# Performance work log

Hardware: AMD Instinct MI355X
Metric: run time of the kernel (lower is better)

Reference implementation:

```python
import jax, jax.numpy as jnp
import numpy as np

N = 50000
IN_C, HID_C, CLS_C = 512, 256, 128
E = 800000


def setup_inputs() -> dict:
    key = jax.random.key(0)
    k1, k2, k3, k4, k5, k6 = jax.random.split(key, 6)
    x = jax.random.normal(k1, (N, IN_C), dtype=jnp.float32)
    edge_index = jax.random.randint(k2, (2, E), 0, N, dtype=jnp.int64)
    # GCNConv params (glorot weights, zero bias as in PyG init)
    W1 = jax.random.normal(k3, (IN_C, HID_C), dtype=jnp.float32) * (1.0 / np.sqrt(IN_C))
    b1 = jnp.zeros((HID_C,), dtype=jnp.float32)
    W2 = jax.random.normal(k4, (HID_C, CLS_C), dtype=jnp.float32) * (1.0 / np.sqrt(HID_C))
    b2 = jnp.zeros((CLS_C,), dtype=jnp.float32)
    return {"x": x, "W1": W1, "b1": b1, "W2": W2, "b2": b2, "edge_index": edge_index}


def _norm_edges(edge_index, n):
    # PyG GCNConv: add self-loops, symmetric normalization deg^-1/2
    loops = jnp.arange(n, dtype=edge_index.dtype)
    src = jnp.concatenate([edge_index[0], loops])
    dst = jnp.concatenate([edge_index[1], loops])
    ones = jnp.ones_like(src, dtype=jnp.float32)
    deg = jax.ops.segment_sum(ones, dst, num_segments=n)
    dinv = jnp.where(deg > 0, jax.lax.rsqrt(deg), 0.0)
    norm = dinv[src] * dinv[dst]  # [E+N]
    return src, dst, norm


def _gcn_conv(x, W, b, src, dst, norm, n):
    h = x @ W  # project first (out_channels < in_channels)
    msg = h[src] * norm[:, None]  # gather + scale, [E+N, C]
    out = jax.ops.segment_sum(msg, dst, num_segments=n)  # scatter-add
    return out + b


def reference(x, W1, b1, W2, b2, edge_index):
    n = x.shape[0]
    src, dst, norm = _norm_edges(edge_index, n)
    h = jax.nn.relu(_gcn_conv(x, W1, b1, src, dst, norm, n))
    # dropout p=0.5 is a no-op in eval mode
    out = _gcn_conv(h, W2, b2, src, dst, norm, n)
    return jax.nn.sigmoid(out)
```

## Files before the change

kernel.cpp:

```cpp
#include <hip/hip_runtime.h>
#include <type_traits>

typedef __attribute__((ext_vector_type(8))) short bf16x8;
typedef __attribute__((ext_vector_type(4))) float f32x4;
typedef unsigned short u16;
typedef unsigned int u32;
typedef __attribute__((address_space(1))) const u32 gu32;
typedef __attribute__((address_space(3))) u32 lu32;

__device__ __forceinline__ float bf2f(u16 u) {
  union { u32 i; float f; } c; c.i = ((u32)u) << 16; return c.f;
}
__device__ __forceinline__ u16 f2bf(float f) {
  union { float f; u32 i; } c; c.f = f;
  u32 u = c.i;
  u32 r = (u + 0x7FFFu + ((u >> 16) & 1u)) >> 16;
  return (u16)r;
}

__device__ __forceinline__ void gld16(const void* g, void* l) {
  __builtin_amdgcn_global_load_lds((gu32*)g, (lu32*)l, 16, 0, 0);
}


__global__ void k_init_deg(int* deg, int n) {
  int i = blockIdx.x * 256 + threadIdx.x;
  if (i < n) deg[i] = 1;
}

__global__ void k_count(const int* __restrict__ ei, int* deg, int E) {
  int e = blockIdx.x * 256 + threadIdx.x;
  if (e < E) atomicAdd(&deg[ei[E + e]], 1);
}

__global__ void k_blocksum(const int* __restrict__ deg, int* bsum, int n) {
  __shared__ int s[256];
  int t = threadIdx.x;
  int i = blockIdx.x * 256 + t;
  s[t] = (i < n) ? (deg[i] - 1) : 0;
  __syncthreads();
  for (int o = 128; o > 0; o >>= 1) {
    if (t < o) s[t] += s[t + o];
    __syncthreads();
  }
  if (t == 0) bsum[blockIdx.x] = s[0];
}

__global__ void k_scanb(const int* __restrict__ bsum, int* bofs, int nb) {
  __shared__ int s[256];
  int t = threadIdx.x;
  int v = (t < nb) ? bsum[t] : 0;
  s[t] = v;
  __syncthreads();
  for (int o = 1; o < 256; o <<= 1) {
    int x = (t >= o) ? s[t - o] : 0;
    __syncthreads();
    s[t] += x;
    __syncthreads();
  }
  bofs[t] = s[t] - v;
}

__global__ void k_rowptr(const int* __restrict__ deg, const int* __restrict__ bofs,
                         int* rowptr, int* cursor, float* dinv, int n) {
  __shared__ int s[256];
  int t = threadIdx.x;
  int i = blockIdx.x * 256 + t;
  int d = (i < n) ? deg[i] : 1;
  int v = (i < n) ? (d - 1) : 0;
  s[t] = v;
  __syncthreads();
  for (int o = 1; o < 256; o <<= 1) {
    int x = (t >= o) ? s[t - o] : 0;
    __syncthreads();
    s[t] += x;
    __syncthreads();
  }
  int excl = s[t] - v + bofs[blockIdx.x];
  if (i < n) {
    rowptr[i] = excl;
    cursor[i] = excl;
    dinv[i] = rsqrtf((float)d);
    if (i == n - 1) rowptr[n] = excl + v;
  }
}

__global__ void k_fill(const int* __restrict__ ei, int* cursor,
                       const float* __restrict__ dinv, int2* colw, int E) {
  int e = blockIdx.x * 256 + threadIdx.x;
  if (e >= E) return;
  int s = ei[e];
  int d = ei[E + e];
  int pos = atomicAdd(&cursor[d], 1);
  colw[pos] = make_int2(s, __float_as_int(dinv[s]));
}

__global__ void k_twt(const float* __restrict__ W, u16* __restrict__ Wt, int K, int N) {
  int i = blockIdx.x * 256 + threadIdx.x;
  if (i >= K * N) return;
  int k = i / N, n = i - k * N;
  Wt[n * K + k] = f2bf(W[i]);
}


template <bool AF32, int K>
__launch_bounds__(256)
__global__ void gemm_kernel(const void* __restrict__ Ap, const u16* __restrict__ Bt,
                            u16* __restrict__ C, int M, int ldc) {
  using AT = typename std::conditional<AF32, float, u16>::type;
  __shared__ AT As_[2][4096];
  __shared__ u16 Bs_[2][4096];

  const int tid = threadIdx.x;
  const int lane = tid & 63;
  const int wid = tid >> 6;
  const int wr = wid >> 1, wc = wid & 1;
  const long brow = (long)blockIdx.x * 128;
  const long bcol = (long)blockIdx.y * 128;

  constexpr int NT = K / 32;
  constexpr int NJA = AF32 ? 4 : 2;

  const AT* agp[NJA];
  AT* alp[NJA];
#pragma unroll
  for (int j = 0; j < NJA; ++j) {
    int idx = j * 256 + tid;
    int row, u;
    if constexpr (AF32) { row = idx >> 3; u = (idx & 7) ^ (row & 7); }
    else                { row = idx >> 2; u = (idx & 3) ^ (row & 3); }
    long grow = brow + row;
    if (grow > (long)M - 1) grow = M - 1;
    agp[j] = (const AT*)Ap + grow * (long)K + u * (AF32 ? 4 : 8);
    alp[j] = &As_[0][idx * (AF32 ? 4 : 8)];
  }
  const u16* bgp[2];
  u16* blp[2];
#pragma unroll
  for (int j = 0; j < 2; ++j) {
    int idx = j * 256 + tid;
    int row = idx >> 2;
    int u = (idx & 3) ^ (row & 3);
    bgp[j] = Bt + (bcol + row) * (long)K + u * 8;
    blp[j] = &Bs_[0][idx * 8];
  }

  f32x4 acc[4][4];
#pragma unroll
  for (int i = 0; i < 4; i++)
#pragma unroll
    for (int j = 0; j < 4; j++) acc[i][j] = (f32x4){0.f, 0.f, 0.f, 0.f};

  auto stage = [&](int kt, int buf) {
    const int boff = buf * 4096;
#pragma unroll
    for (int j = 0; j < NJA; ++j) gld16(agp[j] + kt * 32, alp[j] + boff);
#pragma unroll
    for (int j = 0; j < 2; ++j) gld16(bgp[j] + kt * 32, blp[j] + boff);
  };

  stage(0, 0);
  int cur = 0;
  for (int kt = 0; kt < NT; ++kt) {
    __syncthreads();
    if (kt + 1 < NT) stage(kt + 1, cur ^ 1);

    bf16x8 af[4], bfq[4];
#pragma unroll
    for (int i = 0; i < 4; i++) {
      const int row = wr * 64 + i * 16 + (lane & 15);
      if constexpr (AF32) {
        const float* bp = (const float*)&As_[cur][0] + row * 32;
        const int s = row & 7;
        const int u0 = (lane >> 4) * 2;
        float4 x0 = *(const float4*)(bp + (u0 ^ s) * 4);
        float4 x1 = *(const float4*)(bp + ((u0 + 1) ^ s) * 4);
        union { u32 w[4]; bf16x8 v; } cv;
        asm("v_cvt_pk_bf16_f32 %0, %1, %2" : "=v"(cv.w[0]) : "v"(x0.x), "v"(x0.y));
        asm("v_cvt_pk_bf16_f32 %0, %1, %2" : "=v"(cv.w[1]) : "v"(x0.z), "v"(x0.w));
        asm("v_cvt_pk_bf16_f32 %0, %1, %2" : "=v"(cv.w[2]) : "v"(x1.x), "v"(x1.y));
        asm("v_cvt_pk_bf16_f32 %0, %1, %2" : "=v"(cv.w[3]) : "v"(x1.z), "v"(x1.w));
        af[i] = cv.v;
      } else {
        const int u = (lane >> 4) ^ (row & 3);
        af[i] = *(const bf16x8*)((const u16*)&As_[cur][0] + row * 32 + u * 8);
      }
    }
#pragma unroll
    for (int j = 0; j < 4; j++) {
      const int row = wc * 64 + j * 16 + (lane & 15);
      const int u = (lane >> 4) ^ (row & 3);
      bfq[j] = *(const bf16x8*)(&Bs_[cur][0] + row * 32 + u * 8);
    }
#pragma unroll
    for (int i = 0; i < 4; i++)
#pragma unroll
      for (int j = 0; j < 4; j++)
        acc[i][j] = __builtin_amdgcn_mfma_f32_16x16x32_bf16(af[i], bfq[j], acc[i][j], 0, 0, 0);
    cur ^= 1;
  }

#pragma unroll
  for (int i = 0; i < 4; i++) {
    const long r0 = brow + wr * 64 + i * 16 + ((lane >> 4) * 4);
#pragma unroll
    for (int j = 0; j < 4; j++) {
      const long cc = bcol + wc * 64 + j * 16 + (lane & 15);
#pragma unroll
      for (int q = 0; q < 4; q++) {
        long r = r0 + q;
        if (r < M) C[r * (long)ldc + cc] = f2bf(acc[i][j][q]);
      }
    }
  }
}


__launch_bounds__(256)
__global__ void agg1(const u16* __restrict__ h0, const int* __restrict__ rowptr,
                     const int2* __restrict__ colw, const float* __restrict__ dinv,
                     const float* __restrict__ b1, u16* __restrict__ h, int n) {
  const int wid = threadIdx.x >> 6, lane = threadIdx.x & 63;
  const int node = blockIdx.x * 4 + wid;
  if (node >= n) return;
  const float di = dinv[node];
  ushort4 sv = ((const ushort4*)(h0 + (size_t)node * 256))[lane];
  float a0 = di * bf2f(sv.x), a1 = di * bf2f(sv.y), a2 = di * bf2f(sv.z), a3 = di * bf2f(sv.w);
  int e = rowptr[node];
  const int r1 = rowptr[node + 1];
  for (; e + 4 <= r1; e += 4) {
    int2 c0 = colw[e], c1 = colw[e + 1], c2 = colw[e + 2], c3 = colw[e + 3];
    float w0 = __int_as_float(c0.y), w1 = __int_as_float(c1.y);
    float w2 = __int_as_float(c2.y), w3 = __int_as_float(c3.y);
    ushort4 v0 = ((const ushort4*)(h0 + (size_t)c0.x * 256))[lane];
    ushort4 v1 = ((const ushort4*)(h0 + (size_t)c1.x * 256))[lane];
    ushort4 v2 = ((const ushort4*)(h0 + (size_t)c2.x * 256))[lane];
    ushort4 v3 = ((const ushort4*)(h0 + (size_t)c3.x * 256))[lane];
    a0 += w0 * bf2f(v0.x) + w1 * bf2f(v1.x) + w2 * bf2f(v2.x) + w3 * bf2f(v3.x);
    a1 += w0 * bf2f(v0.y) + w1 * bf2f(v1.y) + w2 * bf2f(v2.y) + w3 * bf2f(v3.y);
    a2 += w0 * bf2f(v0.z) + w1 * bf2f(v1.z) + w2 * bf2f(v2.z) + w3 * bf2f(v3.z);
    a3 += w0 * bf2f(v0.w) + w1 * bf2f(v1.w) + w2 * bf2f(v2.w) + w3 * bf2f(v3.w);
  }
  for (; e < r1; ++e) {
    int2 c = colw[e];
    float wv = __int_as_float(c.y);
    ushort4 v = ((const ushort4*)(h0 + (size_t)c.x * 256))[lane];
    a0 += wv * bf2f(v.x); a1 += wv * bf2f(v.y); a2 += wv * bf2f(v.z); a3 += wv * bf2f(v.w);
  }
  float4 bb = ((const float4*)b1)[lane];
  a0 = a0 * di + bb.x; a1 = a1 * di + bb.y; a2 = a2 * di + bb.z; a3 = a3 * di + bb.w;
  a0 = a0 > 0.f ? a0 : 0.f; a1 = a1 > 0.f ? a1 : 0.f;
  a2 = a2 > 0.f ? a2 : 0.f; a3 = a3 > 0.f ? a3 : 0.f;
  ushort4 o; o.x = f2bf(a0); o.y = f2bf(a1); o.z = f2bf(a2); o.w = f2bf(a3);
  ((ushort4*)(h + (size_t)node * 256))[lane] = o;
}

__device__ __forceinline__ float sigmoidf_(float x) { return 1.f / (1.f + __expf(-x)); }

__launch_bounds__(256)
__global__ void agg2(const u16* __restrict__ h2, const int* __restrict__ rowptr,
                     const int2* __restrict__ colw, const float* __restrict__ dinv,
                     const float* __restrict__ b2, float* __restrict__ out, int n) {
  const int wid = threadIdx.x >> 6, lane = threadIdx.x & 63;
  const int node = blockIdx.x * 4 + wid;
  if (node >= n) return;
  const float di = dinv[node];
  ushort2 sv = ((const ushort2*)(h2 + (size_t)node * 128))[lane];
  float a0 = di * bf2f(sv.x), a1 = di * bf2f(sv.y);
  int e = rowptr[node];
  const int r1 = rowptr[node + 1];
  for (; e + 4 <= r1; e += 4) {
    int2 c0 = colw[e], c1 = colw[e + 1], c2 = colw[e + 2], c3 = colw[e + 3];
    float w0 = __int_as_float(c0.y), w1 = __int_as_float(c1.y);
    float w2 = __int_as_float(c2.y), w3 = __int_as_float(c3.y);
    ushort2 v0 = ((const ushort2*)(h2 + (size_t)c0.x * 128))[lane];
    ushort2 v1 = ((const ushort2*)(h2 + (size_t)c1.x * 128))[lane];
    ushort2 v2 = ((const ushort2*)(h2 + (size_t)c2.x * 128))[lane];
    ushort2 v3 = ((const ushort2*)(h2 + (size_t)c3.x * 128))[lane];
    a0 += w0 * bf2f(v0.x) + w1 * bf2f(v1.x) + w2 * bf2f(v2.x) + w3 * bf2f(v3.x);
    a1 += w0 * bf2f(v0.y) + w1 * bf2f(v1.y) + w2 * bf2f(v2.y) + w3 * bf2f(v3.y);
  }
  for (; e < r1; ++e) {
    int2 c = colw[e];
    float wv = __int_as_float(c.y);
    ushort2 v = ((const ushort2*)(h2 + (size_t)c.x * 128))[lane];
    a0 += wv * bf2f(v.x); a1 += wv * bf2f(v.y);
  }
  float2 bb = ((const float2*)b2)[lane];
  float2 o;
  o.x = sigmoidf_(a0 * di + bb.x);
  o.y = sigmoidf_(a1 * di + bb.y);
  ((float2*)(out + (size_t)node * 128))[lane] = o;
}


extern "C" void kernel_launch(void* const* d_in, const int* in_sizes, int n_in,
                              void* d_out, int out_size, void* d_ws, size_t ws_size,
                              hipStream_t stream) {
  const float* x  = (const float*)d_in[0];
  const float* W1 = (const float*)d_in[1];
  const float* b1 = (const float*)d_in[2];
  const float* W2 = (const float*)d_in[3];
  const float* b2 = (const float*)d_in[4];
  const int*   ei = (const int*)d_in[5];

  const int N = in_sizes[0] / 512;
  const int E = in_sizes[5] / 2;
  const int Mpad = (N + 127) & ~127;
  float* outp = (float*)d_out;

  char* w = (char*)d_ws;
  size_t off = 0;
  auto take = [&](size_t bytes) -> void* {
    void* p = w + off;
    off = (off + bytes + 255) & ~(size_t)255;
    return p;
  };
  u16*   h0     = (u16*)take((size_t)Mpad * 256 * 2);
  u16*   hb     = (u16*)take((size_t)Mpad * 256 * 2);
  u16*   h2     = (u16*)take((size_t)Mpad * 128 * 2);
  u16*   W1t    = (u16*)take(256 * 512 * 2);
  u16*   W2t    = (u16*)take(128 * 256 * 2);
  int*   deg    = (int*)take((size_t)N * 4);
  float* dinv   = (float*)take((size_t)N * 4);
  int*   rowptr = (int*)take((size_t)(N + 1) * 4);
  int*   cursor = (int*)take((size_t)N * 4);
  int2*  colw   = (int2*)take((size_t)E * 8);
  int*   bsum   = (int*)take(256 * 4);
  int*   bofs   = (int*)take(256 * 4);
  (void)ws_size; (void)n_in; (void)out_size;

  const int nb = (N + 255) / 256;
  const int eb = (E + 255) / 256;

  k_init_deg<<<nb, 256, 0, stream>>>(deg, N);
  k_count<<<eb, 256, 0, stream>>>(ei, deg, E);
  k_blocksum<<<nb, 256, 0, stream>>>(deg, bsum, N);
  k_scanb<<<1, 256, 0, stream>>>(bsum, bofs, nb);
  k_rowptr<<<nb, 256, 0, stream>>>(deg, bofs, rowptr, cursor, dinv, N);
  k_fill<<<eb, 256, 0, stream>>>(ei, cursor, dinv, colw, E);
  k_twt<<<(512 * 256 + 255) / 256, 256, 0, stream>>>(W1, W1t, 512, 256);
  k_twt<<<(256 * 128 + 255) / 256, 256, 0, stream>>>(W2, W2t, 256, 128);

  dim3 g1(Mpad / 128, 2);
  gemm_kernel<true, 512><<<g1, 256, 0, stream>>>((const void*)x, W1t, h0, N, 256);
  agg1<<<(N + 3) / 4, 256, 0, stream>>>(h0, rowptr, colw, dinv, b1, hb, N);
  dim3 g2(Mpad / 128, 1);
  gemm_kernel<false, 256><<<g2, 256, 0, stream>>>((const void*)hb, W2t, h2, Mpad, 128);
  agg2<<<(N + 3) / 4, 256, 0, stream>>>(h2, rowptr, colw, dinv, b2, outp, N);
}
```

Measured before the change: 251.9 us.

## Restructure GEMM A-staging to bf16 in LDS and column-split edge aggregation

The first GEMM now loads fp32 A tiles into registers, converts them to bf16 once, and writes them to LDS. This halves LDS footprint and replaces repeated conversions during MFMA fragment reads with a single conversion per tile. The second GEMM uses 64-row tiles to launch more blocks. Both aggregation kernels are replaced by one templated kernel that splits channels into 32-wide partitions across blocks and processes 8 edges in parallel per wave with shuffle reductions. This aims to raise memory-level parallelism and L2 locality for gathers, at the cost of reading the CSR edge lists multiple times (once per partition) and more wasted lanes on low-degree nodes.

```diff
diff --git a/kernel.cpp b/kernel.cpp
--- a/kernel.cpp
+++ b/kernel.cpp
@@ -1,5 +1,4 @@
 #include <hip/hip_runtime.h>
-#include <type_traits>
 
 typedef __attribute__((ext_vector_type(8))) short bf16x8;
 typedef __attribute__((ext_vector_type(4))) float f32x4;
@@ -103,37 +102,25 @@
 }
 
 
-template <bool AF32, int K>
-__launch_bounds__(256)
+template <bool AF32, int K, int BM>
+__launch_bounds__(256, 4)
 __global__ void gemm_kernel(const void* __restrict__ Ap, const u16* __restrict__ Bt,
                             u16* __restrict__ C, int M, int ldc) {
-  using AT = typename std::conditional<AF32, float, u16>::type;
-  __shared__ AT As_[2][4096];
+  constexpr int NT = K / 32;
+  constexpr int AE = BM * 32;
+  constexpr int WROWS = BM / 2;
+  constexpr int FI = WROWS / 16;
+  constexpr int NJA = BM / 64;
+  __shared__ u16 As_[2][AE];
   __shared__ u16 Bs_[2][4096];
 
   const int tid = threadIdx.x;
   const int lane = tid & 63;
   const int wid = tid >> 6;
   const int wr = wid >> 1, wc = wid & 1;
-  const long brow = (long)blockIdx.x * 128;
+  const long brow = (long)blockIdx.x * BM;
   const long bcol = (long)blockIdx.y * 128;
 
-  constexpr int NT = K / 32;
-  constexpr int NJA = AF32 ? 4 : 2;
-
-  const AT* agp[NJA];
-  AT* alp[NJA];
-#pragma unroll
-  for (int j = 0; j < NJA; ++j) {
-    int idx = j * 256 + tid;
-    int row, u;
-    if constexpr (AF32) { row = idx >> 3; u = (idx & 7) ^ (row & 7); }
-    else                { row = idx >> 2; u = (idx & 3) ^ (row & 3); }
-    long grow = brow + row;
-    if (grow > (long)M - 1) grow = M - 1;
-    agp[j] = (const AT*)Ap + grow * (long)K + u * (AF32 ? 4 : 8);
-    alp[j] = &As_[0][idx * (AF32 ? 4 : 8)];
-  }
   const u16* bgp[2];
   u16* blp[2];
 #pragma unroll
@@ -145,64 +132,112 @@
     blp[j] = &Bs_[0][idx * 8];
   }
 
-  f32x4 acc[4][4];
-#pragma unroll
-  for (int i = 0; i < 4; i++)
+  const float* apf = nullptr;
+  int arow = 0, au0 = 0, au1 = 0;
+  const u16* agp[NJA];
+  u16* alp[NJA];
+  if constexpr (AF32) {
+    arow = tid >> 1;
+    int khalf = tid & 1;
+    long grow = brow + arow; if (grow > (long)M - 1) grow = M - 1;
+    apf = (const float*)Ap + grow * (long)K + khalf * 16;
+    int sw = arow & 3;
+    au0 = (2 * khalf) ^ sw;
+    au1 = (2 * khalf + 1) ^ sw;
+  } else {
+#pragma unroll
+    for (int j = 0; j < NJA; ++j) {
+      int idx = j * 256 + tid;
+      int row = idx >> 2;
+      int u = (idx & 3) ^ (row & 3);
+      long grow = brow + row; if (grow > (long)M - 1) grow = M - 1;
+      agp[j] = (const u16*)Ap + grow * (long)K + u * 8;
+      alp[j] = &As_[0][idx * 8];
+    }
+  }
+
+  float4 fa[4];
+  auto loadA = [&](int kt) {
+    const float4* p = (const float4*)(apf + kt * 32);
+#pragma unroll
+    for (int i = 0; i < 4; ++i) fa[i] = p[i];
+  };
+  auto writeA = [&](int buf) {
+    union { u32 w[8]; uint4 v[2]; } pk;
+    asm("v_cvt_pk_bf16_f32 %0, %1, %2" : "=v"(pk.w[0]) : "v"(fa[0].x), "v"(fa[0].y));
+    asm("v_cvt_pk_bf16_f32 %0, %1, %2" : "=v"(pk.w[1]) : "v"(fa[0].z), "v"(fa[0].w));
+    asm("v_cvt_pk_bf16_f32 %0, %1, %2" : "=v"(pk.w[2]) : "v"(fa[1].x), "v"(fa[1].y));
+    asm("v_cvt_pk_bf16_f32 %0, %1, %2" : "=v"(pk.w[3]) : "v"(fa[1].z), "v"(fa[1].w));
+    asm("v_cvt_pk_bf16_f32 %0, %1, %2" : "=v"(pk.w[4]) : "v"(fa[2].x), "v"(fa[2].y));
+    asm("v_cvt_pk_bf16_f32 %0, %1, %2" : "=v"(pk.w[5]) : "v"(fa[2].z), "v"(fa[2].w));
+    asm("v_cvt_pk_bf16_f32 %0, %1, %2" : "=v"(pk.w[6]) : "v"(fa[3].x), "v"(fa[3].y));
+    asm("v_cvt_pk_bf16_f32 %0, %1, %2" : "=v"(pk.w[7]) : "v"(fa[3].z), "v"(fa[3].w));
+    *(uint4*)&As_[buf][arow * 32 + au0 * 8] = pk.v[0];
+    *(uint4*)&As_[buf][arow * 32 + au1 * 8] = pk.v[1];
+  };
+  auto stageB = [&](int kt, int buf) {
+#pragma unroll
+    for (int j = 0; j < 2; ++j) gld16(bgp[j] + kt * 32, blp[j] + buf * 4096);
+  };
+  auto stageAg = [&](int kt, int buf) {
+#pragma unroll
+    for (int j = 0; j < NJA; ++j) gld16(agp[j] + kt * 32, alp[j] + buf * AE);
+  };
+
+  f32x4 acc[FI][4];
+#pragma unroll
+  for (int i = 0; i < FI; i++)
 #pragma unroll
     for (int j = 0; j < 4; j++) acc[i][j] = (f32x4){0.f, 0.f, 0.f, 0.f};
 
-  auto stage = [&](int kt, int buf) {
-    const int boff = buf * 4096;
-#pragma unroll
-    for (int j = 0; j < NJA; ++j) gld16(agp[j] + kt * 32, alp[j] + boff);
-#pragma unroll
-    for (int j = 0; j < 2; ++j) gld16(bgp[j] + kt * 32, blp[j] + boff);
-  };
-
-  stage(0, 0);
+  if constexpr (AF32) {
+    loadA(0);
+    stageB(0, 0);
+    writeA(0);
+  } else {
+    stageAg(0, 0);
+    stageB(0, 0);
+  }
+  __syncthreads();
+
   int cur = 0;
   for (int kt = 0; kt < NT; ++kt) {
-    __syncthreads();
-    if (kt + 1 < NT) stage(kt + 1, cur ^ 1);
-
-    bf16x8 af[4], bfq[4];
-#pragma unroll
-    for (int i = 0; i < 4; i++) {
-      const int row = wr * 64 + i * 16 + (lane & 15);
-      if constexpr (AF32) {
-        const float* bp = (const float*)&As_[cur][0] + row * 32;
-        const int s = row & 7;
-        const int u0 = (lane >> 4) * 2;
-        float4 x0 = *(const float4*)(bp + (u0 ^ s) * 4);
-        float4 x1 = *(const float4*)(bp + ((u0 + 1) ^ s) * 4);
-        union { u32 w[4]; bf16x8 v; } cv;
-        asm("v_cvt_pk_bf16_f32 %0, %1, %2" : "=v"(cv.w[0]) : "v"(x0.x), "v"(x0.y));
-        asm("v_cvt_pk_bf16_f32 %0, %1, %2" : "=v"(cv.w[1]) : "v"(x0.z), "v"(x0.w));
-        asm("v_cvt_pk_bf16_f32 %0, %1, %2" : "=v"(cv.w[2]) : "v"(x1.x), "v"(x1.y));
-        asm("v_cvt_pk_bf16_f32 %0, %1, %2" : "=v"(cv.w[3]) : "v"(x1.z), "v"(x1.w));
-        af[i] = cv.v;
-      } else {
-        const int u = (lane >> 4) ^ (row & 3);
-        af[i] = *(const bf16x8*)((const u16*)&As_[cur][0] + row * 32 + u * 8);
-      }
+    const bool more = (kt + 1 < NT);
+    if constexpr (AF32) {
+      if (more) { loadA(kt + 1); stageB(kt + 1, cur ^ 1); }
+    } else {
+      if (more) { stageAg(kt + 1, cur ^ 1); stageB(kt + 1, cur ^ 1); }
+    }
+
+    bf16x8 af[FI], bfq[4];
+#pragma unroll
+    for (int i = 0; i < FI; i++) {
+      const int row = wr * WROWS + i * 16 + (lane & 15);
+      const int u = (lane >> 4) ^ (row & 3);
+      af[i] = *(const bf16x8*)&As_[cur][row * 32 + u * 8];
     }
 #pragma unroll
     for (int j = 0; j < 4; j++) {
       const int row = wc * 64 + j * 16 + (lane & 15);
       const int u = (lane >> 4) ^ (row & 3);
-      bfq[j] = *(const bf16x8*)(&Bs_[cur][0] + row * 32 + u * 8);
-    }
-#pragma unroll
-    for (int i = 0; i < 4; i++)
+      bfq[j] = *(const bf16x8*)&Bs_[cur][row * 32 + u * 8];
+    }
+#pragma unroll
+    for (int i = 0; i < FI; i++)
 #pragma unroll
       for (int j = 0; j < 4; j++)
         acc[i][j] = __builtin_amdgcn_mfma_f32_16x16x32_bf16(af[i], bfq[j], acc[i][j], 0, 0, 0);
+
+    if constexpr (AF32) {
+      if (more) writeA(cur ^ 1);
+    }
+    __syncthreads();
     cur ^= 1;
   }
 
 #pragma unroll
-  for (int i = 0; i < 4; i++) {
-    const long r0 = brow + wr * 64 + i * 16 + ((lane >> 4) * 4);
+  for (int i = 0; i < FI; i++) {
+    const long r0 = brow + wr * WROWS + i * 16 + ((lane >> 4) * 4);
 #pragma unroll
     for (int j = 0; j < 4; j++) {
       const long cc = bcol + wc * 64 + j * 16 + (lane & 15);
@@ -216,81 +251,62 @@
 }
 
 
+__device__ __forceinline__ float sigmoidf_(float x) { return 1.f / (1.f + __expf(-x)); }
+
+template <int ROWCH, int NP, bool RELU>
 __launch_bounds__(256)
-__global__ void agg1(const u16* __restrict__ h0, const int* __restrict__ rowptr,
-                     const int2* __restrict__ colw, const float* __restrict__ dinv,
-                     const float* __restrict__ b1, u16* __restrict__ h, int n) {
-  const int wid = threadIdx.x >> 6, lane = threadIdx.x & 63;
-  const int node = blockIdx.x * 4 + wid;
-  if (node >= n) return;
-  const float di = dinv[node];
-  ushort4 sv = ((const ushort4*)(h0 + (size_t)node * 256))[lane];
-  float a0 = di * bf2f(sv.x), a1 = di * bf2f(sv.y), a2 = di * bf2f(sv.z), a3 = di * bf2f(sv.w);
-  int e = rowptr[node];
-  const int r1 = rowptr[node + 1];
-  for (; e + 4 <= r1; e += 4) {
-    int2 c0 = colw[e], c1 = colw[e + 1], c2 = colw[e + 2], c3 = colw[e + 3];
-    float w0 = __int_as_float(c0.y), w1 = __int_as_float(c1.y);
-    float w2 = __int_as_float(c2.y), w3 = __int_as_float(c3.y);
-    ushort4 v0 = ((const ushort4*)(h0 + (size_t)c0.x * 256))[lane];
-    ushort4 v1 = ((const ushort4*)(h0 + (size_t)c1.x * 256))[lane];
-    ushort4 v2 = ((const ushort4*)(h0 + (size_t)c2.x * 256))[lane];
-    ushort4 v3 = ((const ushort4*)(h0 + (size_t)c3.x * 256))[lane];
-    a0 += w0 * bf2f(v0.x) + w1 * bf2f(v1.x) + w2 * bf2f(v2.x) + w3 * bf2f(v3.x);
-    a1 += w0 * bf2f(v0.y) + w1 * bf2f(v1.y) + w2 * bf2f(v2.y) + w3 * bf2f(v3.y);
-    a2 += w0 * bf2f(v0.z) + w1 * bf2f(v1.z) + w2 * bf2f(v2.z) + w3 * bf2f(v3.z);
-    a3 += w0 * bf2f(v0.w) + w1 * bf2f(v1.w) + w2 * bf2f(v2.w) + w3 * bf2f(v3.w);
-  }
-  for (; e < r1; ++e) {
-    int2 c = colw[e];
-    float wv = __int_as_float(c.y);
-    ushort4 v = ((const ushort4*)(h0 + (size_t)c.x * 256))[lane];
-    a0 += wv * bf2f(v.x); a1 += wv * bf2f(v.y); a2 += wv * bf2f(v.z); a3 += wv * bf2f(v.w);
-  }
-  float4 bb = ((const float4*)b1)[lane];
-  a0 = a0 * di + bb.x; a1 = a1 * di + bb.y; a2 = a2 * di + bb.z; a3 = a3 * di + bb.w;
-  a0 = a0 > 0.f ? a0 : 0.f; a1 = a1 > 0.f ? a1 : 0.f;
-  a2 = a2 > 0.f ? a2 : 0.f; a3 = a3 > 0.f ? a3 : 0.f;
-  ushort4 o; o.x = f2bf(a0); o.y = f2bf(a1); o.z = f2bf(a2); o.w = f2bf(a3);
-  ((ushort4*)(h + (size_t)node * 256))[lane] = o;
-}
-
-__device__ __forceinline__ float sigmoidf_(float x) { return 1.f / (1.f + __expf(-x)); }
-
-__launch_bounds__(256)
-__global__ void agg2(const u16* __restrict__ h2, const int* __restrict__ rowptr,
-                     const int2* __restrict__ colw, const float* __restrict__ dinv,
-                     const float* __restrict__ b2, float* __restrict__ out, int n) {
-  const int wid = threadIdx.x >> 6, lane = threadIdx.x & 63;
-  const int node = blockIdx.x * 4 + wid;
-  if (node >= n) return;
-  const float di = dinv[node];
-  ushort2 sv = ((const ushort2*)(h2 + (size_t)node * 128))[lane];
-  float a0 = di * bf2f(sv.x), a1 = di * bf2f(sv.y);
-  int e = rowptr[node];
-  const int r1 = rowptr[node + 1];
-  for (; e + 4 <= r1; e += 4) {
-    int2 c0 = colw[e], c1 = colw[e + 1], c2 = colw[e + 2], c3 = colw[e + 3];
-    float w0 = __int_as_float(c0.y), w1 = __int_as_float(c1.y);
-    float w2 = __int_as_float(c2.y), w3 = __int_as_float(c3.y);
-    ushort2 v0 = ((const ushort2*)(h2 + (size_t)c0.x * 128))[lane];
-    ushort2 v1 = ((const ushort2*)(h2 + (size_t)c1.x * 128))[lane];
-    ushort2 v2 = ((const ushort2*)(h2 + (size_t)c2.x * 128))[lane];
-    ushort2 v3 = ((const ushort2*)(h2 + (size_t)c3.x * 128))[lane];
-    a0 += w0 * bf2f(v0.x) + w1 * bf2f(v1.x) + w2 * bf2f(v2.x) + w3 * bf2f(v3.x);
-    a1 += w0 * bf2f(v0.y) + w1 * bf2f(v1.y) + w2 * bf2f(v2.y) + w3 * bf2f(v3.y);
-  }
-  for (; e < r1; ++e) {
-    int2 c = colw[e];
-    float wv = __int_as_float(c.y);
-    ushort2 v = ((const ushort2*)(h2 + (size_t)c.x * 128))[lane];
-    a0 += wv * bf2f(v.x); a1 += wv * bf2f(v.y);
-  }
-  float2 bb = ((const float2*)b2)[lane];
-  float2 o;
-  o.x = sigmoidf_(a0 * di + bb.x);
-  o.y = sigmoidf_(a1 * di + bb.y);
-  ((float2*)(out + (size_t)node * 128))[lane] = o;
+__global__ void agg_kernel(const u16* __restrict__ hin, const int* __restrict__ rowptr,
+                           const int2* __restrict__ colw, const float* __restrict__ dinv,
+                           const float* __restrict__ bias, void* __restrict__ outv, int n) {
+  const int lane = threadIdx.x & 63;
+  const int wid = threadIdx.x >> 6;
+  const int p = blockIdx.x & (NP - 1);
+  const int chunk = blockIdx.x / NP;
+  const int slot = lane >> 3, li = lane & 7;
+  const int choff = (p << 5) + (li << 2);
+
+  for (int i = 0; i < 8; ++i) {
+    const int node = chunk * 32 + wid * 8 + i;
+    if (node >= n) break;
+    const float di = dinv[node];
+    const int r0 = rowptr[node], r1 = rowptr[node + 1];
+    float a0 = 0.f, a1 = 0.f, a2 = 0.f, a3 = 0.f;
+    for (int e0 = r0; e0 < r1; e0 += 8) {
+      int ee = e0 + slot;
+      int ec = ee < r1 ? ee : r1 - 1;
+      int2 c = colw[ec];
+      float w = ee < r1 ? __int_as_float(c.y) : 0.f;
+      const ushort4 v = *(const ushort4*)(hin + (size_t)c.x * ROWCH + choff);
+      a0 += w * bf2f(v.x); a1 += w * bf2f(v.y);
+      a2 += w * bf2f(v.z); a3 += w * bf2f(v.w);
+    }
+    a0 += __shfl_xor(a0, 8);  a1 += __shfl_xor(a1, 8);
+    a2 += __shfl_xor(a2, 8);  a3 += __shfl_xor(a3, 8);
+    a0 += __shfl_xor(a0, 16); a1 += __shfl_xor(a1, 16);
+    a2 += __shfl_xor(a2, 16); a3 += __shfl_xor(a3, 16);
+    a0 += __shfl_xor(a0, 32); a1 += __shfl_xor(a1, 32);
+    a2 += __shfl_xor(a2, 32); a3 += __shfl_xor(a3, 32);
+    if (lane < 8) {
+      const int co = (p << 5) + (lane << 2);
+      const ushort4 sv = *(const ushort4*)(hin + (size_t)node * ROWCH + co);
+      const float dd = di * di;
+      const float4 bb = *(const float4*)(bias + co);
+      float y0 = di * a0 + dd * bf2f(sv.x) + bb.x;
+      float y1 = di * a1 + dd * bf2f(sv.y) + bb.y;
+      float y2 = di * a2 + dd * bf2f(sv.z) + bb.z;
+      float y3 = di * a3 + dd * bf2f(sv.w) + bb.w;
+      if constexpr (RELU) {
+        y0 = fmaxf(y0, 0.f); y1 = fmaxf(y1, 0.f);
+        y2 = fmaxf(y2, 0.f); y3 = fmaxf(y3, 0.f);
+        ushort4 ov;
+        ov.x = f2bf(y0); ov.y = f2bf(y1); ov.z = f2bf(y2); ov.w = f2bf(y3);
+        *(ushort4*)((u16*)outv + (size_t)node * ROWCH + co) = ov;
+      } else {
+        *(float4*)((float*)outv + (size_t)node * ROWCH + co) =
+            make_float4(sigmoidf_(y0), sigmoidf_(y1), sigmoidf_(y2), sigmoidf_(y3));
+      }
+    }
+  }
 }
 
 
@@ -342,10 +358,12 @@
   k_twt<<<(512 * 256 + 255) / 256, 256, 0, stream>>>(W1, W1t, 512, 256);
   k_twt<<<(256 * 128 + 255) / 256, 256, 0, stream>>>(W2, W2t, 256, 128);
 
+  const int chunks = (N + 31) / 32;
+
   dim3 g1(Mpad / 128, 2);
-  gemm_kernel<true, 512><<<g1, 256, 0, stream>>>((const void*)x, W1t, h0, N, 256);
-  agg1<<<(N + 3) / 4, 256, 0, stream>>>(h0, rowptr, colw, dinv, b1, hb, N);
-  dim3 g2(Mpad / 128, 1);
-  gemm_kernel<false, 256><<<g2, 256, 0, stream>>>((const void*)hb, W2t, h2, Mpad, 128);
-  agg2<<<(N + 3) / 4, 256, 0, stream>>>(h2, rowptr, colw, dinv, b2, outp, N);
-}
+  gemm_kernel<true, 512, 128><<<g1, 256, 0, stream>>>((const void*)x, W1t, h0, N, 256);
+  agg_kernel<256, 8, true><<<chunks * 8, 256, 0, stream>>>(h0, rowptr, colw, dinv, b1, hb, N);
+  dim3 g2(Mpad / 64, 1);
+  gemm_kernel<false, 256, 64><<<g2, 256, 0, stream>>>((const void*)hb, W2t, h2, Mpad, 128);
+  agg_kernel<128, 4, false><<<chunks * 4, 256, 0, stream>>>(h2, rowptr, colw, dinv, b2, outp, N);
+}
```

After: 411.2 us. 1.63x slower.
